# Kernel optimization log

Hardware: AMD Instinct MI355X
Metric: run time of the kernel (lower is better)

Reference implementation:

```python
import jax, jax.numpy as jnp
import numpy as np

H, D, DK, DV = 8, 512, 64, 64
B, L = 2, 2048
LN_EPS = 1e-5


def setup_inputs() -> dict:
    key = jax.random.key(0)
    ks = jax.random.split(key, 12)
    q = jax.random.normal(ks[0], (B, L, D), jnp.float32)
    k = jax.random.normal(ks[1], (B, L, D), jnp.float32)
    v = jax.random.normal(ks[2], (B, L, D), jnp.float32)
    mask = jax.random.randint(ks[3], (H * B, L, L), 0, 2) > 0
    sq = np.sqrt(2.0 / (D + DK)).astype(np.float32)
    sv = np.sqrt(2.0 / (D + DV)).astype(np.float32)
    Wq = jax.random.normal(ks[4], (H * DK, D), jnp.float32) * sq
    Wk = jax.random.normal(ks[5], (H * DK, D), jnp.float32) * sq
    Wv = jax.random.normal(ks[6], (H * DV, D), jnp.float32) * sv
    xav = np.sqrt(2.0 / (H * DV + D)).astype(np.float32)
    Wfc = jax.random.normal(ks[7], (D, H * DV), jnp.float32) * xav
    bfc = jnp.zeros((D,), jnp.float32)
    gamma = jnp.ones((D,), jnp.float32)
    beta = jnp.zeros((D,), jnp.float32)
    return {"q": q, "k": k, "v": v, "mask": mask, "Wq": Wq, "Wk": Wk,
            "Wv": Wv, "Wfc": Wfc, "bfc": bfc, "gamma": gamma, "beta": beta}


def reference(q, k, v, mask, Wq, Wk, Wv, Wfc, bfc, gamma, beta):
    # dropout in eval mode (identity)
    temperature = jnp.sqrt(jnp.asarray(DK, q.dtype))
    residual = q
    # projections -> (H, B, L, dk/dv), matching permute(2,0,1,3)
    qh = (q @ Wq.T).reshape(B, L, H, DK).transpose(2, 0, 1, 3)
    kh = (k @ Wk.T).reshape(B, L, H, DK).transpose(2, 0, 1, 3)
    vh = (v @ Wv.T).reshape(B, L, H, DV).transpose(2, 0, 1, 3)
    attn = jnp.einsum('hbqd,hbkd->hbqk', qh, kh) / temperature
    m = mask.reshape(H, B, L, L)
    attn = jnp.where(m, jnp.asarray(-1e10, attn.dtype), attn)
    attn = jax.nn.softmax(attn, axis=-1)
    out = jnp.einsum('hbqk,hbkd->hbqd', attn, vh)  # (H,B,L,DV)
    out = out.transpose(1, 2, 0, 3).reshape(B, L, H * DV)
    out = out @ Wfc.T + bfc
    x = out + residual
    mu = jnp.mean(x, axis=-1, keepdims=True)
    var = jnp.var(x, axis=-1, keepdims=True)
    return gamma * (x - mu) * jax.lax.rsqrt(var + LN_EPS) + beta
```

## Files before the change

kernel.cpp:

```cpp
#include <hip/hip_runtime.h>
#include <hip/hip_bf16.h>
#include <cmath>
#include <cstdint>

#define H_ 8
#define B_ 2
#define L_ 2048
#define D_ 512
#define SPLIT_ 4

typedef __attribute__((ext_vector_type(8))) short short8_t;
typedef __attribute__((ext_vector_type(4))) float float4_t;
typedef __attribute__((ext_vector_type(4))) unsigned short ushort4_t;
typedef __attribute__((ext_vector_type(2))) unsigned int uint2_t;
typedef __attribute__((ext_vector_type(4))) unsigned int uint4_t;

__device__ __forceinline__ unsigned short bf16u(float f) {
  union { __hip_bfloat16 b; unsigned short u; } c;
  c.b = __float2bfloat16(f);
  return c.u;
}
__device__ __forceinline__ unsigned bf16x2(float lo, float hi) {
  return (unsigned)bf16u(lo) | ((unsigned)bf16u(hi) << 16);
}

__device__ __forceinline__ unsigned pack8(unsigned long long x) {
  x |= x >> 4; x |= x >> 2; x |= x >> 1;
  x &= 0x0101010101010101ULL;
  return (unsigned)((x * 0x0102040810204080ULL) >> 56);
}

__global__ __launch_bounds__(256)
void cvt_w(const float* __restrict__ wfc, unsigned short* __restrict__ wfcb) {
  int i = (blockIdx.x * 256 + threadIdx.x) * 4;
  float4_t a = *(const float4_t*)(wfc + i);
  ushort4_t o;
  o[0] = bf16u(a[0]); o[1] = bf16u(a[1]); o[2] = bf16u(a[2]); o[3] = bf16u(a[3]);
  *(ushort4_t*)(wfcb + i) = o;
}

__global__ __launch_bounds__(512)
void proj_gemm(const float* __restrict__ q, const float* __restrict__ k,
               const float* __restrict__ v,
               const float* __restrict__ wq, const float* __restrict__ wk,
               const float* __restrict__ wv,
               unsigned short* __restrict__ Qp, unsigned short* __restrict__ Kp,
               unsigned short* __restrict__ Vt) {
  __shared__ unsigned short As[128][72];
  __shared__ unsigned short Bs[64][72];
  const int tid = threadIdx.x, lane = tid & 63, wave = tid >> 6;
  const int g = lane >> 4, qi = lane & 15;
  const int m0 = blockIdx.x * 128, n0 = blockIdx.y * 64;
  const int z = blockIdx.z;
  const float* A = (z == 0) ? q : (z == 1) ? k : v;
  const float* W = (z == 0) ? wq : (z == 1) ? wk : wv;

  float4_t acc[4] = {};
  const int ar = tid >> 2, ac = (tid & 3) * 16;
  const int br = tid >> 3, bc = (tid & 7) * 8;

  for (int kt = 0; kt < 512; kt += 64) {
    const float* src = A + (size_t)(m0 + ar) * 512 + kt + ac;
    float4_t f0 = *(const float4_t*)(src);
    float4_t f1 = *(const float4_t*)(src + 4);
    float4_t f2 = *(const float4_t*)(src + 8);
    float4_t f3 = *(const float4_t*)(src + 12);
    short8_t s0, s1;
    s0[0] = bf16u(f0[0]); s0[1] = bf16u(f0[1]); s0[2] = bf16u(f0[2]); s0[3] = bf16u(f0[3]);
    s0[4] = bf16u(f1[0]); s0[5] = bf16u(f1[1]); s0[6] = bf16u(f1[2]); s0[7] = bf16u(f1[3]);
    s1[0] = bf16u(f2[0]); s1[1] = bf16u(f2[1]); s1[2] = bf16u(f2[2]); s1[3] = bf16u(f2[3]);
    s1[4] = bf16u(f3[0]); s1[5] = bf16u(f3[1]); s1[6] = bf16u(f3[2]); s1[7] = bf16u(f3[3]);
    *(short8_t*)(&As[ar][ac]) = s0;
    *(short8_t*)(&As[ar][ac + 8]) = s1;
    const float* wsrc = W + (size_t)(n0 + br) * 512 + kt + bc;
    float4_t w0 = *(const float4_t*)(wsrc);
    float4_t w1 = *(const float4_t*)(wsrc + 4);
    short8_t sw;
    sw[0] = bf16u(w0[0]); sw[1] = bf16u(w0[1]); sw[2] = bf16u(w0[2]); sw[3] = bf16u(w0[3]);
    sw[4] = bf16u(w1[0]); sw[5] = bf16u(w1[1]); sw[6] = bf16u(w1[2]); sw[7] = bf16u(w1[3]);
    *(short8_t*)(&Bs[br][bc]) = sw;
    __syncthreads();
#pragma unroll
    for (int kk = 0; kk < 2; kk++) {
      const int krow = kk * 32 + g * 8;
      short8_t a = *(const short8_t*)(&As[wave * 16 + qi][krow]);
#pragma unroll
      for (int n = 0; n < 4; n++) {
        short8_t b = *(const short8_t*)(&Bs[n * 16 + qi][krow]);
        acc[n] = __builtin_amdgcn_mfma_f32_16x16x32_bf16(a, b, acc[n], 0, 0, 0);
      }
    }
    __syncthreads();
  }

  const int gmb = m0 + wave * 16 + g * 4;
#pragma unroll
  for (int n = 0; n < 4; n++) {
    int gn = n0 + n * 16 + qi;
    int h = gn >> 6, d = gn & 63;
    if (z == 2) {
      int bb = gmb >> 11, l = gmb & 2047;
      ushort4_t o;
#pragma unroll
      for (int r = 0; r < 4; r++) o[r] = bf16u(acc[n][r]);
      *(ushort4_t*)(Vt + ((size_t)(h * B_ + bb) * 64 + d) * L_ + l) = o;
    } else {
      float sc = (z == 0) ? 0.125f : 1.0f;
      unsigned short* O = (z == 0) ? Qp : Kp;
#pragma unroll
      for (int r = 0; r < 4; r++) {
        int gm = gmb + r;
        int bb = gm >> 11, l = gm & 2047;
        O[((size_t)(h * B_ + bb) * L_ + l) * 64 + d] = bf16u(acc[n][r] * sc);
      }
    }
  }
}

template<int MS>
__device__ __forceinline__ void attn_body(
    const unsigned short* __restrict__ Qp, const unsigned short* __restrict__ Kp,
    const unsigned short* __restrict__ Vt, const unsigned char* __restrict__ mask,
    float* __restrict__ Opart, float* __restrict__ MLpart,
    unsigned short (*Ks)[72], unsigned short (*Vs)[72], unsigned int (*Ps)[36]) {
  const int tid = threadIdx.x, lane = tid & 63, wave = tid >> 6;
  const int g = lane >> 4, qi = lane & 15;
  const int hb = blockIdx.y;
  const int sp = blockIdx.z;
  const int k_begin = sp * (L_ / SPLIT_), k_end = k_begin + L_ / SPLIT_;
  const int qg0 = blockIdx.x * 64 + wave * 16;
  const int qg = qg0 + qi;
  const size_t base = (size_t)hb * (L_ * 64);

  const size_t mrowoff = ((size_t)hb * L_ + qg0 + (lane >> 2)) * L_;
  const unsigned char* mb1 = mask + mrowoff + (lane & 3) * 16;
  const unsigned* mb4 = (const unsigned*)mask + mrowoff + (lane & 3) * 16;

  short8_t qf[2];
#pragma unroll
  for (int kk = 0; kk < 2; kk++)
    qf[kk] = *(const short8_t*)(Qp + base + (size_t)qg * 64 + kk * 32 + g * 8);

  float4_t o[4] = {};
  float mrun = -INFINITY, lrun = 0.f;
  const int sr = tid >> 3, sc = (tid & 7) * 8;
  const int srcA = qi * 4;

  short8_t kr0, kr1, vr0, vr1;
  unsigned fb;
  {
    const int k0 = k_begin;
    kr0 = *(const short8_t*)(Kp + base + (size_t)(k0 + sr) * 64 + sc);
    kr1 = *(const short8_t*)(Kp + base + (size_t)(k0 + sr + 32) * 64 + sc);
    vr0 = *(const short8_t*)(Vt + base + (size_t)sr * L_ + k0 + sc);
    vr1 = *(const short8_t*)(Vt + base + (size_t)(sr + 32) * L_ + k0 + sc);
    if (MS == 1) {
      uint4_t x = *(const uint4_t*)(mb1 + k0);
      unsigned long long lo = ((unsigned long long)x[1] << 32) | x[0];
      unsigned long long hi = ((unsigned long long)x[3] << 32) | x[2];
      fb = pack8(lo) | (pack8(hi) << 8);
    } else {
      fb = 0;
#pragma unroll
      for (int j = 0; j < 4; j++) {
        uint4_t x = *(const uint4_t*)(mb4 + k0 + j * 4);
        fb |= (((unsigned)(x[0] != 0)) | ((unsigned)(x[1] != 0) << 1) |
               ((unsigned)(x[2] != 0) << 2) | ((unsigned)(x[3] != 0) << 3)) << (j * 4);
      }
    }
  }

  for (int k0 = k_begin; k0 < k_end; k0 += 64) {
    *(short8_t*)(&Ks[sr][sc]) = kr0;
    *(short8_t*)(&Ks[sr + 32][sc]) = kr1;
    *(short8_t*)(&Vs[sr][sc]) = vr0;
    *(short8_t*)(&Vs[sr + 32][sc]) = vr1;
    unsigned fb_cur = fb;
    __syncthreads();

    if (k0 + 64 < k_end) {
      const int kn = k0 + 64;
      kr0 = *(const short8_t*)(Kp + base + (size_t)(kn + sr) * 64 + sc);
      kr1 = *(const short8_t*)(Kp + base + (size_t)(kn + sr + 32) * 64 + sc);
      vr0 = *(const short8_t*)(Vt + base + (size_t)sr * L_ + kn + sc);
      vr1 = *(const short8_t*)(Vt + base + (size_t)(sr + 32) * L_ + kn + sc);
      if (MS == 1) {
        uint4_t x = *(const uint4_t*)(mb1 + kn);
        unsigned long long lo = ((unsigned long long)x[1] << 32) | x[0];
        unsigned long long hi = ((unsigned long long)x[3] << 32) | x[2];
        fb = pack8(lo) | (pack8(hi) << 8);
      } else {
        fb = 0;
#pragma unroll
        for (int j = 0; j < 4; j++) {
          uint4_t x = *(const uint4_t*)(mb4 + kn + j * 4);
          fb |= (((unsigned)(x[0] != 0)) | ((unsigned)(x[1] != 0) << 1) |
                 ((unsigned)(x[2] != 0) << 2) | ((unsigned)(x[3] != 0) << 3)) << (j * 4);
        }
      }
    }

    unsigned nib[4];
#pragma unroll
    for (int t = 0; t < 4; t++)
      nib[t] = ((unsigned)__shfl((int)fb_cur, srcA + t, 64) >> (g * 4)) & 0xFu;

    float4_t st[4] = {};
#pragma unroll
    for (int kk = 0; kk < 2; kk++) {
      const int krow = kk * 32 + g * 8;
#pragma unroll
      for (int t = 0; t < 4; t++) {
        short8_t a = *(const short8_t*)(&Ks[t * 16 + qi][krow]);
        st[t] = __builtin_amdgcn_mfma_f32_16x16x32_bf16(a, qf[kk], st[t], 0, 0, 0);
      }
    }

    float tmax = -INFINITY;
#pragma unroll
    for (int t = 0; t < 4; t++)
#pragma unroll
      for (int r = 0; r < 4; r++) {
        if ((nib[t] >> r) & 1u) st[t][r] = -1e10f;
        tmax = fmaxf(tmax, st[t][r]);
      }
    tmax = fmaxf(tmax, __shfl_xor(tmax, 16, 64));
    tmax = fmaxf(tmax, __shfl_xor(tmax, 32, 64));

    float nm = fmaxf(mrun, tmax);
    float fac = __expf(mrun - nm);
    mrun = nm;

    float psum = 0.f;
    unsigned w8[4][2];
#pragma unroll
    for (int t = 0; t < 4; t++) {
      float p0 = __expf(st[t][0] - nm);
      float p1 = __expf(st[t][1] - nm);
      float p2 = __expf(st[t][2] - nm);
      float p3 = __expf(st[t][3] - nm);
      psum += (p0 + p1) + (p2 + p3);
      w8[t][0] = bf16x2(p0, p1);
      w8[t][1] = bf16x2(p2, p3);
    }
    psum += __shfl_xor(psum, 16, 64);
    psum += __shfl_xor(psum, 32, 64);
    lrun = lrun * fac + psum;
#pragma unroll
    for (int n2 = 0; n2 < 4; n2++)
#pragma unroll
      for (int r = 0; r < 4; r++) o[n2][r] *= fac;

#pragma unroll
    for (int t = 0; t < 4; t++) {
      uint2_t w2; w2[0] = w8[t][0]; w2[1] = w8[t][1];
      *(uint2_t*)(&Ps[qi][t * 8 + g * 2]) = w2;
    }
#pragma unroll
    for (int s = 0; s < 2; s++) {
      short8_t pb = *(const short8_t*)(&Ps[qi][s * 16 + g * 4]);
#pragma unroll
      for (int n2 = 0; n2 < 4; n2++) {
        short8_t a = *(const short8_t*)(&Vs[n2 * 16 + qi][s * 32 + g * 8]);
        o[n2] = __builtin_amdgcn_mfma_f32_16x16x32_bf16(a, pb, o[n2], 0, 0, 0);
      }
    }
    __syncthreads();
  }

  const size_t pb = (((size_t)sp * 16 + hb) * L_ + qg) * 64;
#pragma unroll
  for (int n2 = 0; n2 < 4; n2++)
    *(float4_t*)(Opart + pb + n2 * 16 + g * 4) = o[n2];
  if (lane < 16) {
    float* ml = MLpart + (((size_t)sp * 16 + hb) * L_ + qg) * 2;
    ml[0] = mrun; ml[1] = lrun;
  }
}

__global__ __launch_bounds__(256)
void attn_split(const unsigned short* __restrict__ Qp, const unsigned short* __restrict__ Kp,
                const unsigned short* __restrict__ Vt, const unsigned char* __restrict__ mask,
                float* __restrict__ Opart, float* __restrict__ MLpart) {
  __shared__ unsigned short Ks[64][72];
  __shared__ unsigned short Vs[64][72];
  __shared__ unsigned int PsAll[4][16][36];
  const int wave = threadIdx.x >> 6;
  unsigned probe = ((const unsigned*)mask)[threadIdx.x & 63];
  if (__any(probe > 1u))
    attn_body<1>(Qp, Kp, Vt, mask, Opart, MLpart, Ks, Vs, PsAll[wave]);
  else
    attn_body<4>(Qp, Kp, Vt, mask, Opart, MLpart, Ks, Vs, PsAll[wave]);
}

__global__ __launch_bounds__(256)
void attn_combine(const float* __restrict__ Opart, const float* __restrict__ MLpart,
                  unsigned short* __restrict__ Y) {
  int gid = blockIdx.x * 256 + threadIdx.x;
  int dvc = (gid & 7) * 8;
  int hbq = gid >> 3;
  int hb = hbq >> 11, qq = hbq & 2047;
  int h = hb >> 1, bb = hb & 1;
  float m[SPLIT_], l[SPLIT_];
  float M = -INFINITY;
#pragma unroll
  for (int s = 0; s < SPLIT_; s++) {
    const float* ml = MLpart + (((size_t)s * 16 + hb) * L_ + qq) * 2;
    m[s] = ml[0]; l[s] = ml[1];
    M = fmaxf(M, m[s]);
  }
  float denom = 0.f, e[SPLIT_];
#pragma unroll
  for (int s = 0; s < SPLIT_; s++) { e[s] = __expf(m[s] - M); denom += l[s] * e[s]; }
  float inv = 1.0f / denom;
  float acc[8] = {};
#pragma unroll
  for (int s = 0; s < SPLIT_; s++) {
    const float* p = Opart + (((size_t)s * 16 + hb) * L_ + qq) * 64 + dvc;
    float4_t a0 = *(const float4_t*)(p);
    float4_t a1 = *(const float4_t*)(p + 4);
    float w = e[s] * inv;
#pragma unroll
    for (int j = 0; j < 4; j++) { acc[j] += a0[j] * w; acc[j + 4] += a1[j] * w; }
  }
  short8_t ov;
#pragma unroll
  for (int j = 0; j < 8; j++) ov[j] = bf16u(acc[j]);
  *(short8_t*)(Y + ((size_t)(bb * L_ + qq)) * 512 + h * 64 + dvc) = ov;
}

__global__ __launch_bounds__(512)
void fc_gemm(const unsigned short* __restrict__ Yb, const unsigned short* __restrict__ wfcb,
             const float* __restrict__ resid, const float* __restrict__ bfc,
             float* __restrict__ out) {
  __shared__ unsigned short As[128][72];
  __shared__ unsigned short Bs[64][72];
  const int tid = threadIdx.x, lane = tid & 63, wave = tid >> 6;
  const int g = lane >> 4, qi = lane & 15;
  const int m0 = blockIdx.x * 128, n0 = blockIdx.y * 64;
  float4_t acc[4] = {};
  const int ar = tid >> 2, ac = (tid & 3) * 16;
  const int br = tid >> 3, bc = (tid & 7) * 8;

  for (int kt = 0; kt < 512; kt += 64) {
    const unsigned short* src = Yb + (size_t)(m0 + ar) * 512 + kt + ac;
    *(short8_t*)(&As[ar][ac]) = *(const short8_t*)(src);
    *(short8_t*)(&As[ar][ac + 8]) = *(const short8_t*)(src + 8);
    *(short8_t*)(&Bs[br][bc]) = *(const short8_t*)(wfcb + (size_t)(n0 + br) * 512 + kt + bc);
    __syncthreads();
#pragma unroll
    for (int kk = 0; kk < 2; kk++) {
      const int krow = kk * 32 + g * 8;
      short8_t a = *(const short8_t*)(&As[wave * 16 + qi][krow]);
#pragma unroll
      for (int n = 0; n < 4; n++) {
        short8_t b = *(const short8_t*)(&Bs[n * 16 + qi][krow]);
        acc[n] = __builtin_amdgcn_mfma_f32_16x16x32_bf16(a, b, acc[n], 0, 0, 0);
      }
    }
    __syncthreads();
  }

  const int gmb = m0 + wave * 16 + g * 4;
#pragma unroll
  for (int n = 0; n < 4; n++) {
    int gn = n0 + n * 16 + qi;
    float bv = bfc[gn];
#pragma unroll
    for (int r = 0; r < 4; r++) {
      int gm = gmb + r;
      out[(size_t)gm * 512 + gn] = acc[n][r] + bv + resid[(size_t)gm * 512 + gn];
    }
  }
}

__global__ __launch_bounds__(256)
void ln_kernel(float* __restrict__ Z, const float* __restrict__ gamma,
               const float* __restrict__ beta) {
  const int row = blockIdx.x * 4 + (threadIdx.x >> 6);
  const int lane = threadIdx.x & 63;
  float* zp = Z + (size_t)row * 512 + lane * 8;
  float4_t x0 = *(const float4_t*)(zp);
  float4_t x1 = *(const float4_t*)(zp + 4);
  float s = 0.f, s2 = 0.f;
#pragma unroll
  for (int j = 0; j < 4; j++) { s += x0[j] + x1[j]; s2 += x0[j] * x0[j] + x1[j] * x1[j]; }
#pragma unroll
  for (int mm = 1; mm < 64; mm <<= 1) { s += __shfl_xor(s, mm, 64); s2 += __shfl_xor(s2, mm, 64); }
  float mu = s * (1.f / 512.f);
  float var = s2 * (1.f / 512.f) - mu * mu;
  float inv = rsqrtf(var + 1e-5f);
  float4_t g0 = *(const float4_t*)(gamma + lane * 8);
  float4_t g1 = *(const float4_t*)(gamma + lane * 8 + 4);
  float4_t b0 = *(const float4_t*)(beta + lane * 8);
  float4_t b1 = *(const float4_t*)(beta + lane * 8 + 4);
#pragma unroll
  for (int j = 0; j < 4; j++) {
    x0[j] = g0[j] * (x0[j] - mu) * inv + b0[j];
    x1[j] = g1[j] * (x1[j] - mu) * inv + b1[j];
  }
  *(float4_t*)(zp) = x0;
  *(float4_t*)(zp + 4) = x1;
}

extern "C" void kernel_launch(void* const* d_in, const int* in_sizes, int n_in,
                              void* d_out, int out_size, void* d_ws, size_t ws_size,
                              hipStream_t stream) {
  const float* q   = (const float*)d_in[0];
  const float* k   = (const float*)d_in[1];
  const float* v   = (const float*)d_in[2];
  const unsigned char* mask = (const unsigned char*)d_in[3];
  const float* Wq  = (const float*)d_in[4];
  const float* Wk  = (const float*)d_in[5];
  const float* Wv  = (const float*)d_in[6];
  const float* Wfc = (const float*)d_in[7];
  const float* bfc = (const float*)d_in[8];
  const float* gamma = (const float*)d_in[9];
  const float* beta  = (const float*)d_in[10];
  float* out = (float*)d_out;

  char* ws = (char*)d_ws;
  unsigned short* wfcb = (unsigned short*)(ws);
  unsigned short* Qp   = wfcb + 262144;
  unsigned short* Kp   = Qp + 2097152;
  unsigned short* Vt   = Kp + 2097152;
  unsigned short* Y    = Vt + 2097152;
  float* Opart         = (float*)(Y + 2097152);
  float* MLpart        = Opart + (size_t)SPLIT_ * 16 * L_ * 64;

  cvt_w<<<256, 256, 0, stream>>>(Wfc, wfcb);
  proj_gemm<<<dim3(32, 8, 3), 512, 0, stream>>>(q, k, v, Wq, Wk, Wv, Qp, Kp, Vt);
  attn_split<<<dim3(32, 16, SPLIT_), 256, 0, stream>>>(Qp, Kp, Vt, mask, Opart, MLpart);
  attn_combine<<<1024, 256, 0, stream>>>(Opart, MLpart, Y);
  fc_gemm<<<dim3(32, 8), 512, 0, stream>>>(Y, wfcb, q, bfc, out);
  ln_kernel<<<1024, 256, 0, stream>>>(out, gamma, beta);
}
```

Before: 136.7 us.

## Double attention block query tile to 128 and store partial outputs in bf16

The attention split kernel now runs 8 waves per block covering 128 queries, so each K/V tile staged in shared memory is reused by twice as many queries. Each thread loads one K row chunk and one V row chunk instead of two. Partial outputs are written as bf16 instead of fp32, which halves the traffic between the split and combine kernels. The trade-offs are fewer blocks in the grid (1024), more register and LDS pressure per block, and some extra rounding in the partial outputs.

```diff
diff --git a/kernel.cpp b/kernel.cpp
--- a/kernel.cpp
+++ b/kernel.cpp
@@ -22,6 +22,9 @@
 }
 __device__ __forceinline__ unsigned bf16x2(float lo, float hi) {
   return (unsigned)bf16u(lo) | ((unsigned)bf16u(hi) << 16);
+}
+__device__ __forceinline__ float bf2f(unsigned short u) {
+  union { unsigned u; float f; } c; c.u = (unsigned)u << 16; return c.f;
 }
 
 __device__ __forceinline__ unsigned pack8(unsigned long long x) {
@@ -121,14 +124,14 @@
 __device__ __forceinline__ void attn_body(
     const unsigned short* __restrict__ Qp, const unsigned short* __restrict__ Kp,
     const unsigned short* __restrict__ Vt, const unsigned char* __restrict__ mask,
-    float* __restrict__ Opart, float* __restrict__ MLpart,
+    unsigned short* __restrict__ Opart, float* __restrict__ MLpart,
     unsigned short (*Ks)[72], unsigned short (*Vs)[72], unsigned int (*Ps)[36]) {
   const int tid = threadIdx.x, lane = tid & 63, wave = tid >> 6;
   const int g = lane >> 4, qi = lane & 15;
   const int hb = blockIdx.y;
   const int sp = blockIdx.z;
   const int k_begin = sp * (L_ / SPLIT_), k_end = k_begin + L_ / SPLIT_;
-  const int qg0 = blockIdx.x * 64 + wave * 16;
+  const int qg0 = blockIdx.x * 128 + wave * 16;
   const int qg = qg0 + qi;
   const size_t base = (size_t)hb * (L_ * 64);
 
@@ -146,14 +149,12 @@
   const int sr = tid >> 3, sc = (tid & 7) * 8;
   const int srcA = qi * 4;
 
-  short8_t kr0, kr1, vr0, vr1;
+  short8_t kr, vr;
   unsigned fb;
   {
     const int k0 = k_begin;
-    kr0 = *(const short8_t*)(Kp + base + (size_t)(k0 + sr) * 64 + sc);
-    kr1 = *(const short8_t*)(Kp + base + (size_t)(k0 + sr + 32) * 64 + sc);
-    vr0 = *(const short8_t*)(Vt + base + (size_t)sr * L_ + k0 + sc);
-    vr1 = *(const short8_t*)(Vt + base + (size_t)(sr + 32) * L_ + k0 + sc);
+    kr = *(const short8_t*)(Kp + base + (size_t)(k0 + sr) * 64 + sc);
+    vr = *(const short8_t*)(Vt + base + (size_t)sr * L_ + k0 + sc);
     if (MS == 1) {
       uint4_t x = *(const uint4_t*)(mb1 + k0);
       unsigned long long lo = ((unsigned long long)x[1] << 32) | x[0];
@@ -171,19 +172,15 @@
   }
 
   for (int k0 = k_begin; k0 < k_end; k0 += 64) {
-    *(short8_t*)(&Ks[sr][sc]) = kr0;
-    *(short8_t*)(&Ks[sr + 32][sc]) = kr1;
-    *(short8_t*)(&Vs[sr][sc]) = vr0;
-    *(short8_t*)(&Vs[sr + 32][sc]) = vr1;
+    *(short8_t*)(&Ks[sr][sc]) = kr;
+    *(short8_t*)(&Vs[sr][sc]) = vr;
     unsigned fb_cur = fb;
     __syncthreads();
 
     if (k0 + 64 < k_end) {
       const int kn = k0 + 64;
-      kr0 = *(const short8_t*)(Kp + base + (size_t)(kn + sr) * 64 + sc);
-      kr1 = *(const short8_t*)(Kp + base + (size_t)(kn + sr + 32) * 64 + sc);
-      vr0 = *(const short8_t*)(Vt + base + (size_t)sr * L_ + kn + sc);
-      vr1 = *(const short8_t*)(Vt + base + (size_t)(sr + 32) * L_ + kn + sc);
+      kr = *(const short8_t*)(Kp + base + (size_t)(kn + sr) * 64 + sc);
+      vr = *(const short8_t*)(Vt + base + (size_t)sr * L_ + kn + sc);
       if (MS == 1) {
         uint4_t x = *(const uint4_t*)(mb1 + kn);
         unsigned long long lo = ((unsigned long long)x[1] << 32) | x[0];
@@ -270,21 +267,25 @@
 
   const size_t pb = (((size_t)sp * 16 + hb) * L_ + qg) * 64;
 #pragma unroll
-  for (int n2 = 0; n2 < 4; n2++)
-    *(float4_t*)(Opart + pb + n2 * 16 + g * 4) = o[n2];
+  for (int n2 = 0; n2 < 4; n2++) {
+    ushort4_t ov;
+#pragma unroll
+    for (int r = 0; r < 4; r++) ov[r] = bf16u(o[n2][r]);
+    *(ushort4_t*)(Opart + pb + n2 * 16 + g * 4) = ov;
+  }
   if (lane < 16) {
     float* ml = MLpart + (((size_t)sp * 16 + hb) * L_ + qg) * 2;
     ml[0] = mrun; ml[1] = lrun;
   }
 }
 
-__global__ __launch_bounds__(256)
+__global__ __launch_bounds__(512)
 void attn_split(const unsigned short* __restrict__ Qp, const unsigned short* __restrict__ Kp,
                 const unsigned short* __restrict__ Vt, const unsigned char* __restrict__ mask,
-                float* __restrict__ Opart, float* __restrict__ MLpart) {
+                unsigned short* __restrict__ Opart, float* __restrict__ MLpart) {
   __shared__ unsigned short Ks[64][72];
   __shared__ unsigned short Vs[64][72];
-  __shared__ unsigned int PsAll[4][16][36];
+  __shared__ unsigned int PsAll[8][16][36];
   const int wave = threadIdx.x >> 6;
   unsigned probe = ((const unsigned*)mask)[threadIdx.x & 63];
   if (__any(probe > 1u))
@@ -294,7 +295,7 @@
 }
 
 __global__ __launch_bounds__(256)
-void attn_combine(const float* __restrict__ Opart, const float* __restrict__ MLpart,
+void attn_combine(const unsigned short* __restrict__ Opart, const float* __restrict__ MLpart,
                   unsigned short* __restrict__ Y) {
   int gid = blockIdx.x * 256 + threadIdx.x;
   int dvc = (gid & 7) * 8;
@@ -316,12 +317,15 @@
   float acc[8] = {};
 #pragma unroll
   for (int s = 0; s < SPLIT_; s++) {
-    const float* p = Opart + (((size_t)s * 16 + hb) * L_ + qq) * 64 + dvc;
-    float4_t a0 = *(const float4_t*)(p);
-    float4_t a1 = *(const float4_t*)(p + 4);
+    const unsigned short* p = Opart + (((size_t)s * 16 + hb) * L_ + qq) * 64 + dvc;
+    ushort4_t a0 = *(const ushort4_t*)(p);
+    ushort4_t a1 = *(const ushort4_t*)(p + 4);
     float w = e[s] * inv;
 #pragma unroll
-    for (int j = 0; j < 4; j++) { acc[j] += a0[j] * w; acc[j + 4] += a1[j] * w; }
+    for (int j = 0; j < 4; j++) {
+      acc[j] += bf2f(a0[j]) * w;
+      acc[j + 4] += bf2f(a1[j]) * w;
+    }
   }
   short8_t ov;
 #pragma unroll
@@ -425,12 +429,12 @@
   unsigned short* Kp   = Qp + 2097152;
   unsigned short* Vt   = Kp + 2097152;
   unsigned short* Y    = Vt + 2097152;
-  float* Opart         = (float*)(Y + 2097152);
-  float* MLpart        = Opart + (size_t)SPLIT_ * 16 * L_ * 64;
+  unsigned short* Opart = Y + 2097152;
+  float* MLpart = (float*)(Opart + (size_t)SPLIT_ * 16 * L_ * 64);
 
   cvt_w<<<256, 256, 0, stream>>>(Wfc, wfcb);
   proj_gemm<<<dim3(32, 8, 3), 512, 0, stream>>>(q, k, v, Wq, Wk, Wv, Qp, Kp, Vt);
-  attn_split<<<dim3(32, 16, SPLIT_), 256, 0, stream>>>(Qp, Kp, Vt, mask, Opart, MLpart);
+  attn_split<<<dim3(16, 16, SPLIT_), 512, 0, stream>>>(Qp, Kp, Vt, mask, Opart, MLpart);
   attn_combine<<<1024, 256, 0, stream>>>(Opart, MLpart, Y);
   fc_gemm<<<dim3(32, 8), 512, 0, stream>>>(Y, wfcb, q, bfc, out);
   ln_kernel<<<1024, 256, 0, stream>>>(out, gamma, beta);
```

Result: faster. 127.6 us (-6.7%).
